# Kernel optimization log

Measured on AMD Instinct MI355X. Metric: run time of the kernel, lower is better.

## Reference

```python
import jax, jax.numpy as jnp
import numpy as np
from jax import lax

B, P, E, H, V, S = 128, 196, 2048, 512, 10000, 21


def setup_inputs() -> dict:
    key = jax.random.key(0)
    ks = jax.random.split(key, 16)
    r = lambda k, shape, s=0.02: (jax.random.normal(k, shape, jnp.float32) * s)
    return {
        "img_features": jax.random.normal(ks[0], (B, P, E), jnp.float32),
        "captions": jax.random.randint(ks[1], (B, S), 0, V),
        "U_w": r(ks[2], (H, H)), "U_b": jnp.zeros((H,), jnp.float32),
        "W_w": r(ks[3], (E, H)), "W_b": jnp.zeros((H,), jnp.float32),
        "v_w": r(ks[4], (H, 1)), "v_b": jnp.zeros((1,), jnp.float32),
        "init_h_w": r(ks[5], (E, H)), "init_h_b": jnp.zeros((H,), jnp.float32),
        "init_c_w": r(ks[6], (E, H)), "init_c_b": jnp.zeros((H,), jnp.float32),
        "f_beta_w": r(ks[7], (H, E)), "f_beta_b": jnp.zeros((E,), jnp.float32),
        "out_w": r(ks[8], (H, V)), "out_b": jnp.zeros((V,), jnp.float32),
        "emb": r(ks[9], (V, H)),
        "lstm_Wih": r(ks[10], (H + E, 4 * H)), "lstm_Whh": r(ks[11], (H, 4 * H)),
        "lstm_bih": jnp.zeros((4 * H,), jnp.float32), "lstm_bhh": jnp.zeros((4 * H,), jnp.float32),
    }


def reference(img_features, captions, U_w, U_b, W_w, W_b, v_w, v_b,
              init_h_w, init_h_b, init_c_w, init_c_b, f_beta_w, f_beta_b,
              out_w, out_b, emb, lstm_Wih, lstm_Whh, lstm_bih, lstm_bhh):
    batch = img_features.shape[0]
    T = captions.shape[1] - 1  # max_timespan (static)

    # init LSTM state from mean-pooled image features
    avg = img_features.mean(axis=1)                       # [B, E]
    h0 = jnp.tanh(avg @ init_h_w + init_h_b)              # [B, H]
    c0 = jnp.tanh(avg @ init_c_w + init_c_b)              # [B, H]

    # precompute W(img_features) once; it does not depend on h
    W_s = img_features @ W_w + W_b                        # [B, P, H]

    # in training mode the original feeds the embedding of word 0 every step
    emb0 = jnp.broadcast_to(emb[0], (batch, emb.shape[1]))  # [B, H]

    def step(carry, _):
        h, c = carry
        # additive attention
        att = jnp.tanh(W_s + (h @ U_w + U_b)[:, None, :])      # [B, P, H]
        e = (att @ v_w)[..., 0] + v_b[0]                        # [B, P]
        alpha = jax.nn.softmax(e, axis=1)                       # [B, P]
        context = jnp.einsum('bp,bpe->be', alpha, img_features) # [B, E]
        # gated context
        gate = jax.nn.sigmoid(h @ f_beta_w + f_beta_b)          # [B, E]
        x = jnp.concatenate([emb0, gate * context], axis=1)     # [B, H+E]
        # LSTMCell (torch gate order i, f, g, o)
        gates = x @ lstm_Wih + lstm_bih + h @ lstm_Whh + lstm_bhh  # [B, 4H]
        i, f, g, o = jnp.split(gates, 4, axis=1)
        i = jax.nn.sigmoid(i); f = jax.nn.sigmoid(f)
        g = jnp.tanh(g); o = jax.nn.sigmoid(o)
        c_new = f * c + i * g
        h_new = o * jnp.tanh(c_new)
        out = h_new @ out_w + out_b                             # [B, V] (dropout = identity, eval)
        return (h_new, c_new), (out, alpha)

    (_, _), (preds, alphas) = lax.scan(step, (h0, c0), None, length=T)
    preds = jnp.transpose(preds, (1, 0, 2))    # [B, T, V]
    alphas = jnp.transpose(alphas, (1, 0, 2))  # [B, T, P]
    return preds, alphas
```

## Files before the change

### kernel.cpp

```cpp
#include <hip/hip_runtime.h>
#include <stdint.h>


typedef unsigned short u16;
typedef unsigned int u32;
typedef __attribute__((ext_vector_type(8))) short bf16x8;
typedef __attribute__((ext_vector_type(4))) float f32x4;

__device__ __forceinline__ float bf2f(u16 u) { return __uint_as_float(((u32)u) << 16); }
__device__ __forceinline__ u16 f2bf(float f) {
  u32 x = __float_as_uint(f);
  u32 r = x + 0x7fffu + ((x >> 16) & 1u);
  return (u16)(r >> 16);
}
__device__ __forceinline__ float tanh_f(float x) {
  x = fminf(15.f, fmaxf(-15.f, x));
  float e = __expf(2.f * x);
  return 1.f - 2.f * __builtin_amdgcn_rcpf(e + 1.f);
}
__device__ __forceinline__ float sigm_f(float x) {
  x = fminf(30.f, fmaxf(-30.f, x));
  return __builtin_amdgcn_rcpf(1.f + __expf(-x));
}

__global__ __launch_bounds__(256) void k_f32_to_bf16(const float* __restrict__ in,
                                                     u16* __restrict__ out) {
  size_t i = ((size_t)blockIdx.x * 256 + threadIdx.x) * 8;
  float4 v0 = *(const float4*)(in + i);
  float4 v1 = *(const float4*)(in + i + 4);
  union { u16 u[8]; uint4 v; } r;
  r.u[0] = f2bf(v0.x); r.u[1] = f2bf(v0.y); r.u[2] = f2bf(v0.z); r.u[3] = f2bf(v0.w);
  r.u[4] = f2bf(v1.x); r.u[5] = f2bf(v1.y); r.u[6] = f2bf(v1.z); r.u[7] = f2bf(v1.w);
  *(uint4*)(out + i) = r.v;
}

__global__ __launch_bounds__(256) void k_avg(const u16* __restrict__ imgb,
                                             u16* __restrict__ avgb) {
  int b = blockIdx.y;
  int c0 = blockIdx.x * 512 + threadIdx.x * 2;
  const u32* p0 = (const u32*)(imgb + (size_t)b * 196 * 2048 + c0);
  float s0 = 0.f, s1 = 0.f;
  for (int p = 0; p < 196; ++p) {
    u32 v = p0[(size_t)p * 1024];
    s0 += bf2f((u16)(v & 0xffff));
    s1 += bf2f((u16)(v >> 16));
  }
  const float inv = 1.f / 196.f;
  u32 o = ((u32)f2bf(s1 * inv) << 16) | (u32)f2bf(s0 * inv);
  *(u32*)(avgb + (size_t)b * 2048 + c0) = o;
}

template <bool PERM>
__global__ __launch_bounds__(256) void k_transpose_bf16(const float* __restrict__ in,
                                                        int R, int C, int Cpad,
                                                        u16* __restrict__ out, int out_ld) {
  __shared__ float tile[32][33];
  int c0 = blockIdx.x * 32, r0 = blockIdx.y * 32;
  int tx = threadIdx.x, ty = threadIdx.y;
#pragma unroll
  for (int i = 0; i < 32; i += 8) {
    int r = r0 + ty + i, c = c0 + tx;
    tile[ty + i][tx] = (r < R && c < C) ? in[(size_t)r * C + c] : 0.f;
  }
  __syncthreads();
#pragma unroll
  for (int i = 0; i < 32; i += 8) {
    int c = c0 + ty + i, r = r0 + tx;
    if (c < Cpad && r < R) {
      int co = PERM ? ((c & 511) * 4 + (c >> 9)) : c;
      out[(size_t)co * out_ld + r] = f2bf(tile[tx][ty + i]);
    }
  }
}

__global__ __launch_bounds__(256) void k_cbias(const float* __restrict__ emb,
                                               const float* __restrict__ Wih,
                                               const float* __restrict__ bih,
                                               const float* __restrict__ bhh,
                                               float* __restrict__ cb) {
  __shared__ float e0[512];
  int tid = threadIdx.x;
  for (int i = tid; i < 512; i += 256) e0[i] = emb[i];
  __syncthreads();
  int n = blockIdx.x * 256 + tid;
  float s = bih[n] + bhh[n];
  for (int k = 0; k < 512; ++k) s += e0[k] * Wih[(size_t)k * 2048 + n];
  cb[(n & 511) * 4 + (n >> 9)] = s;
}

enum { EPI_TANH_H = 0, EPI_TANH_C, EPI_GATE, EPI_LSTM };

template <int EPI>
__global__ __launch_bounds__(256) void k_gemm64(
    const u16* __restrict__ A, const u16* __restrict__ BT, int K, int Ntiles,
    const float* __restrict__ bias, float* __restrict__ outF,
    u16* __restrict__ outB, u16* __restrict__ outB2, u16* __restrict__ outB3,
    const float* __restrict__ ctx, int tstep) {
  __shared__ __align__(16) u16 Asm[64 * 72];
  __shared__ __align__(16) u16 Bsm[64 * 72];
  int bid = blockIdx.x;
  int mt = bid / Ntiles, nt = bid % Ntiles;
  long m0 = (long)mt * 64, n0 = (long)nt * 64;
  int tid = threadIdx.x, lane = tid & 63, w = tid >> 6;
  int srow = tid >> 3, schk = tid & 7;
  f32x4 acc[4] = {};
  const u16* Ap0 = A + (m0 + srow) * K + schk * 8;
  const u16* Ap1 = A + (m0 + srow + 32) * K + schk * 8;
  const u16* Bp0 = BT + (n0 + srow) * K + schk * 8;
  const u16* Bp1 = BT + (n0 + srow + 32) * K + schk * 8;
  u16* Aw0 = Asm + srow * 72 + schk * 8;
  u16* Aw1 = Asm + (srow + 32) * 72 + schk * 8;
  u16* Bw0 = Bsm + srow * 72 + schk * 8;
  u16* Bw1 = Bsm + (srow + 32) * 72 + schk * 8;
  const u16* Ar = Asm + (w * 16 + (lane & 15)) * 72 + (lane >> 4) * 8;
  const u16* Br = Bsm + (lane & 15) * 72 + (lane >> 4) * 8;
  for (int k0 = 0; k0 < K; k0 += 64) {
    uint4 a0 = *(const uint4*)(Ap0 + k0);
    uint4 a1 = *(const uint4*)(Ap1 + k0);
    uint4 b0 = *(const uint4*)(Bp0 + k0);
    uint4 b1 = *(const uint4*)(Bp1 + k0);
    __syncthreads();
    *(uint4*)Aw0 = a0;
    *(uint4*)Aw1 = a1;
    *(uint4*)Bw0 = b0;
    *(uint4*)Bw1 = b1;
    __syncthreads();
#pragma unroll
    for (int kk = 0; kk < 2; ++kk) {
      bf16x8 af = *(const bf16x8*)(Ar + kk * 32);
#pragma unroll
      for (int sn = 0; sn < 4; ++sn) {
        bf16x8 bfr = *(const bf16x8*)(Br + sn * 16 * 72 + kk * 32);
        acc[sn] = __builtin_amdgcn_mfma_f32_16x16x32_bf16(af, bfr, acc[sn], 0, 0, 0);
      }
    }
  }
  int cb = lane & 15, rb = (lane >> 4) * 4;
  if constexpr (EPI == EPI_LSTM) {
    __shared__ float gtile[64][68];
#pragma unroll
    for (int sn = 0; sn < 4; ++sn)
#pragma unroll
      for (int r = 0; r < 4; ++r)
        gtile[w * 16 + rb + r][sn * 16 + cb] = acc[sn][r] + bias[n0 + sn * 16 + cb];
    __syncthreads();
#pragma unroll
    for (int i = 0; i < 4; ++i) {
      int idx = tid * 4 + i;
      int m = idx >> 4, chl = idx & 15;
      float iv = gtile[m][chl * 4 + 0];
      float fv = gtile[m][chl * 4 + 1];
      float gv = gtile[m][chl * 4 + 2];
      float ov = gtile[m][chl * 4 + 3];
      long bg = m0 + m;
      int ch = (int)(n0 >> 2) + chl;
      long ci = bg * 512 + ch;
      float cn = sigm_f(fv) * outF[ci] + sigm_f(iv) * tanh_f(gv);
      float h = sigm_f(ov) * tanh_f(cn);
      outF[ci] = cn;
      u16 hv = f2bf(h);
      outB[ci] = hv;
      outB2[bg * 2560 + 2048 + ch] = hv;
      outB3[((long)tstep * 128 + bg) * 512 + ch] = hv;
    }
  } else {
#pragma unroll
    for (int sn = 0; sn < 4; ++sn) {
#pragma unroll
      for (int r = 0; r < 4; ++r) {
        long m = m0 + w * 16 + rb + r;
        long n = n0 + sn * 16 + cb;
        float v = acc[sn][r];
        if (EPI == EPI_TANH_H) {
          u16 hv = f2bf(tanh_f(v + bias[n]));
          outB[m * 512 + n] = hv;
          outB2[m * 2560 + 2048 + n] = hv;
        } else if (EPI == EPI_TANH_C) {
          outF[m * 512 + n] = tanh_f(v + bias[n]);
        } else {
          outB[m * 2560 + n] = f2bf(sigm_f(v + bias[n]) * ctx[m * 2048 + n]);
        }
      }
    }
  }
}

enum { EPI128_WS = 0, EPI128_OUT };

template <int EPI>
__global__ __launch_bounds__(256) void k_gemm128(
    const u16* __restrict__ A, const u16* __restrict__ BT, int K, int Ntiles,
    const float* __restrict__ bias, float* __restrict__ outF,
    u16* __restrict__ outB, int ncap) {
  __shared__ __align__(16) u16 Asm[128 * 72];
  __shared__ __align__(16) u16 Bsm[128 * 72];
  int bid = blockIdx.x;
  int mt = bid / Ntiles, nt = bid % Ntiles;
  long m0 = (long)mt * 128, n0 = (long)nt * 128;
  int tid = threadIdx.x, lane = tid & 63, w = tid >> 6;
  int wr = w >> 1, wc = w & 1;
  int srow = tid >> 3, schk = tid & 7;
  f32x4 acc[4][4] = {};
  const u16* Ap = A + (m0 + srow) * K + schk * 8;
  const u16* Bp = BT + (n0 + srow) * K + schk * 8;
  u16* Aw = Asm + srow * 72 + schk * 8;
  u16* Bw = Bsm + srow * 72 + schk * 8;
  const u16* Ar = Asm + (wr * 64 + (lane & 15)) * 72 + (lane >> 4) * 8;
  const u16* Br = Bsm + (wc * 64 + (lane & 15)) * 72 + (lane >> 4) * 8;
  for (int k0 = 0; k0 < K; k0 += 64) {
    uint4 a0 = *(const uint4*)(Ap + k0);
    uint4 a1 = *(const uint4*)(Ap + (size_t)32 * K + k0);
    uint4 a2 = *(const uint4*)(Ap + (size_t)64 * K + k0);
    uint4 a3 = *(const uint4*)(Ap + (size_t)96 * K + k0);
    uint4 b0 = *(const uint4*)(Bp + k0);
    uint4 b1 = *(const uint4*)(Bp + (size_t)32 * K + k0);
    uint4 b2 = *(const uint4*)(Bp + (size_t)64 * K + k0);
    uint4 b3 = *(const uint4*)(Bp + (size_t)96 * K + k0);
    __syncthreads();
    *(uint4*)Aw = a0;
    *(uint4*)(Aw + 32 * 72) = a1;
    *(uint4*)(Aw + 64 * 72) = a2;
    *(uint4*)(Aw + 96 * 72) = a3;
    *(uint4*)Bw = b0;
    *(uint4*)(Bw + 32 * 72) = b1;
    *(uint4*)(Bw + 64 * 72) = b2;
    *(uint4*)(Bw + 96 * 72) = b3;
    __syncthreads();
#pragma unroll
    for (int kk = 0; kk < 2; ++kk) {
      bf16x8 af[4], bfv[4];
#pragma unroll
      for (int i = 0; i < 4; ++i) {
        af[i] = *(const bf16x8*)(Ar + i * 16 * 72 + kk * 32);
        bfv[i] = *(const bf16x8*)(Br + i * 16 * 72 + kk * 32);
      }
#pragma unroll
      for (int sm = 0; sm < 4; ++sm)
#pragma unroll
        for (int sn = 0; sn < 4; ++sn)
          acc[sm][sn] = __builtin_amdgcn_mfma_f32_16x16x32_bf16(af[sm], bfv[sn],
                                                                acc[sm][sn], 0, 0, 0);
    }
  }
  int cb = lane & 15, rb = (lane >> 4) * 4;
#pragma unroll
  for (int sm = 0; sm < 4; ++sm) {
#pragma unroll
    for (int sn = 0; sn < 4; ++sn) {
#pragma unroll
      for (int r = 0; r < 4; ++r) {
        long m = m0 + wr * 64 + sm * 16 + rb + r;
        long n = n0 + wc * 64 + sn * 16 + cb;
        float v = acc[sm][sn][r];
        if (EPI == EPI128_WS) {
          outB[m * 512 + n] = f2bf(v + bias[n]);
        } else {
          if (n < ncap) {
            long t = m >> 7, b = m & 127;
            outF[b * 200000 + t * 10000 + n] = v + bias[n];
          }
        }
      }
    }
  }
}

__global__ __launch_bounds__(512) void k_attn_ctx(
    const u16* __restrict__ hb, const u16* __restrict__ UwB,
    const float* __restrict__ U_b, const float* __restrict__ v_w,
    const u16* __restrict__ WsB, const u16* __restrict__ imgb,
    float* __restrict__ ctx, float* __restrict__ alphas_t) {
  int b = blockIdx.x, tid = threadIdx.x, lane = tid & 63, w = tid >> 6;
  __shared__ float h_s[512], hu_s[512], v_s[512], al_s[200];
  h_s[tid] = bf2f(hb[b * 512 + tid]);
  v_s[tid] = v_w[tid];
  __syncthreads();
  {
    float s = U_b[tid];
    const u16* up = UwB + tid;
#pragma unroll 8
    for (int k = 0; k < 512; ++k) s += h_s[k] * bf2f(up[(size_t)k * 512]);
    hu_s[tid] = s;
  }
  __syncthreads();
  for (int p = w; p < 196; p += 8) {
    uint4 pk = *(const uint4*)(WsB + ((size_t)b * 196 + p) * 512 + lane * 8);
    const u16* u = (const u16*)&pk;
    float e = 0.f;
#pragma unroll
    for (int j = 0; j < 8; ++j) {
      int hch = lane * 8 + j;
      e += tanh_f(bf2f(u[j]) + hu_s[hch]) * v_s[hch];
    }
#pragma unroll
    for (int off = 32; off; off >>= 1) e += __shfl_xor(e, off);
    if (lane == 0) al_s[p] = e;
  }
  __syncthreads();
  if (w == 0) {
    float mx = -1e30f;
    for (int q = lane; q < 196; q += 64) mx = fmaxf(mx, al_s[q]);
#pragma unroll
    for (int off = 32; off; off >>= 1) mx = fmaxf(mx, __shfl_xor(mx, off));
    float ssum = 0.f;
    for (int q = lane; q < 196; q += 64) {
      float ex = __expf(al_s[q] - mx);
      al_s[q] = ex;
      ssum += ex;
    }
#pragma unroll
    for (int off = 32; off; off >>= 1) ssum += __shfl_xor(ssum, off);
    float inv = 1.f / ssum;
    for (int q = lane; q < 196; q += 64) al_s[q] *= inv;
  }
  __syncthreads();
  if (tid < 196) alphas_t[(size_t)b * 3920 + tid] = al_s[tid];
  const u32* ib = (const u32*)(imgb + (size_t)b * 196 * 2048) + tid;
  float a0 = 0.f, a1 = 0.f, a2 = 0.f, a3 = 0.f;
#pragma unroll 2
  for (int p = 0; p < 196; ++p) {
    float ap = al_s[p];
    u32 v0 = ib[(size_t)p * 1024];
    u32 v1 = ib[(size_t)p * 1024 + 512];
    a0 += ap * bf2f((u16)(v0 & 0xffff));
    a1 += ap * bf2f((u16)(v0 >> 16));
    a2 += ap * bf2f((u16)(v1 & 0xffff));
    a3 += ap * bf2f((u16)(v1 >> 16));
  }
  float* cp = ctx + (size_t)b * 2048;
  cp[tid * 2] = a0;
  cp[tid * 2 + 1] = a1;
  cp[1024 + tid * 2] = a2;
  cp[1024 + tid * 2 + 1] = a3;
}

extern "C" void kernel_launch(void* const* d_in, const int* in_sizes, int n_in,
                              void* d_out, int out_size, void* d_ws, size_t ws_size,
                              hipStream_t stream) {
  const float* img = (const float*)d_in[0];
  const float* U_w = (const float*)d_in[2];
  const float* U_b = (const float*)d_in[3];
  const float* W_w = (const float*)d_in[4];
  const float* W_b = (const float*)d_in[5];
  const float* v_w = (const float*)d_in[6];
  const float* ih_w = (const float*)d_in[8];
  const float* ih_b = (const float*)d_in[9];
  const float* ic_w = (const float*)d_in[10];
  const float* ic_b = (const float*)d_in[11];
  const float* fb_w = (const float*)d_in[12];
  const float* fb_b = (const float*)d_in[13];
  const float* out_w = (const float*)d_in[14];
  const float* out_b = (const float*)d_in[15];
  const float* emb = (const float*)d_in[16];
  const float* Wih = (const float*)d_in[17];
  const float* Whh = (const float*)d_in[18];
  const float* bih = (const float*)d_in[19];
  const float* bhh = (const float*)d_in[20];
  float* preds = (float*)d_out;
  float* alphas = (float*)d_out + 25600000;

  char* ws = (char*)d_ws;
  size_t off = 0;
  auto alloc = [&](size_t bytes) {
    void* p = ws + off;
    off = (off + bytes + 255) & ~(size_t)255;
    return p;
  };
  u16* imgb = (u16*)alloc((size_t)128 * 196 * 2048 * 2);
  u16* avgb = (u16*)alloc((size_t)128 * 2048 * 2);
  u16* WsB = (u16*)alloc((size_t)128 * 196 * 512 * 2);
  u16* WwT = (u16*)alloc((size_t)512 * 2048 * 2);
  u16* UwB = (u16*)alloc((size_t)512 * 512 * 2);
  u16* ihT = (u16*)alloc((size_t)512 * 2048 * 2);
  u16* icT = (u16*)alloc((size_t)512 * 2048 * 2);
  u16* fbT = (u16*)alloc((size_t)2048 * 512 * 2);
  u16* WcT = (u16*)alloc((size_t)2048 * 2560 * 2);
  u16* owT = (u16*)alloc((size_t)10112 * 512 * 2);
  float* cbias = (float*)alloc(2048 * 4);
  u16* hb = (u16*)alloc((size_t)128 * 512 * 2);
  float* cbuf = (float*)alloc((size_t)128 * 512 * 4);
  float* ctx = (float*)alloc((size_t)128 * 2048 * 4);
  u16* AbufA = (u16*)alloc((size_t)128 * 2560 * 2);
  u16* AbufB = (u16*)alloc((size_t)128 * 2560 * 2);
  u16* hAll = (u16*)alloc((size_t)2560 * 512 * 2);
  if (off > ws_size) return;
  (void)in_sizes; (void)n_in; (void)out_size;

  dim3 tb(32, 8);
  k_f32_to_bf16<<<25088, 256, 0, stream>>>(img, imgb);
  k_f32_to_bf16<<<128, 256, 0, stream>>>(U_w, UwB);
  k_avg<<<dim3(4, 128), 256, 0, stream>>>(imgb, avgb);
  k_transpose_bf16<false><<<dim3(16, 64), tb, 0, stream>>>(W_w, 2048, 512, 512, WwT, 2048);
  k_transpose_bf16<false><<<dim3(16, 64), tb, 0, stream>>>(ih_w, 2048, 512, 512, ihT, 2048);
  k_transpose_bf16<false><<<dim3(16, 64), tb, 0, stream>>>(ic_w, 2048, 512, 512, icT, 2048);
  k_transpose_bf16<false><<<dim3(64, 16), tb, 0, stream>>>(fb_w, 512, 2048, 2048, fbT, 512);
  k_transpose_bf16<false><<<dim3(316, 16), tb, 0, stream>>>(out_w, 512, 10000, 10112, owT, 512);
  k_transpose_bf16<true><<<dim3(64, 64), tb, 0, stream>>>(Wih + 512 * 2048, 2048, 2048, 2048, WcT, 2560);
  k_transpose_bf16<true><<<dim3(64, 16), tb, 0, stream>>>(Whh, 512, 2048, 2048, WcT + 2048, 2560);
  k_cbias<<<8, 256, 0, stream>>>(emb, Wih, bih, bhh, cbias);
  k_gemm128<EPI128_WS><<<784, 256, 0, stream>>>(imgb, WwT, 2048, 4, W_b, nullptr, WsB, 0);
  k_gemm64<EPI_TANH_H><<<16, 256, 0, stream>>>(avgb, ihT, 2048, 8, ih_b, nullptr, hb,
                                               AbufA, nullptr, nullptr, 0);
  k_gemm64<EPI_TANH_C><<<16, 256, 0, stream>>>(avgb, icT, 2048, 8, ic_b, cbuf, nullptr,
                                               nullptr, nullptr, nullptr, 0);

  for (int t = 0; t < 20; ++t) {
    u16* Acur = (t & 1) ? AbufB : AbufA;
    u16* Anxt = (t & 1) ? AbufA : AbufB;
    k_attn_ctx<<<128, 512, 0, stream>>>(hb, UwB, U_b, v_w, WsB, imgb, ctx,
                                        alphas + (size_t)t * 196);
    k_gemm64<EPI_GATE><<<64, 256, 0, stream>>>(hb, fbT, 512, 32, fb_b, nullptr, Acur,
                                               nullptr, nullptr, ctx, 0);
    k_gemm64<EPI_LSTM><<<64, 256, 0, stream>>>(Acur, WcT, 2560, 32, cbias, cbuf, hb,
                                               Anxt, hAll, nullptr, t);
  }
  k_gemm128<EPI128_OUT><<<20 * 79, 256, 0, stream>>>(hAll, owT, 512, 79, out_b,
                                                     preds, nullptr, 10000);
}
```

Baseline: 2.833 ms.

## Merge attention, gate and h@Whh GEMMs into two kernels per timestep

Each timestep's three launches become two. The first kernel runs, in separate blocks, the per-batch attention/context work and an MFMA GEMM of h against a concatenated [f_beta | Whh] weight. The second kernel fuses the sigmoid-gate times context into the A-operand load of the context@Wih GEMM, then adds the precomputed h@Whh and runs the LSTM cell epilogue. Alongside this, the attention path is restructured to use vectorized loads split across waves with shared-memory partial reductions. The aim is fewer launches and less serial latency on the recurrent critical path, at the cost of an fp32 intermediate buffer and sigmoid work recomputed per N-tile.

```diff
diff --git a/kernel.cpp b/kernel.cpp
--- a/kernel.cpp
+++ b/kernel.cpp
@@ -88,14 +88,12 @@
   cb[(n & 511) * 4 + (n >> 9)] = s;
 }
 
-enum { EPI_TANH_H = 0, EPI_TANH_C, EPI_GATE, EPI_LSTM };
+enum { EPI_TANH_H = 0, EPI_TANH_C };
 
 template <int EPI>
 __global__ __launch_bounds__(256) void k_gemm64(
     const u16* __restrict__ A, const u16* __restrict__ BT, int K, int Ntiles,
-    const float* __restrict__ bias, float* __restrict__ outF,
-    u16* __restrict__ outB, u16* __restrict__ outB2, u16* __restrict__ outB3,
-    const float* __restrict__ ctx, int tstep) {
+    const float* __restrict__ bias, float* __restrict__ outF, u16* __restrict__ outB) {
   __shared__ __align__(16) u16 Asm[64 * 72];
   __shared__ __align__(16) u16 Bsm[64 * 72];
   int bid = blockIdx.x;
@@ -136,51 +134,15 @@
     }
   }
   int cb = lane & 15, rb = (lane >> 4) * 4;
-  if constexpr (EPI == EPI_LSTM) {
-    __shared__ float gtile[64][68];
-#pragma unroll
-    for (int sn = 0; sn < 4; ++sn)
-#pragma unroll
-      for (int r = 0; r < 4; ++r)
-        gtile[w * 16 + rb + r][sn * 16 + cb] = acc[sn][r] + bias[n0 + sn * 16 + cb];
-    __syncthreads();
-#pragma unroll
-    for (int i = 0; i < 4; ++i) {
-      int idx = tid * 4 + i;
-      int m = idx >> 4, chl = idx & 15;
-      float iv = gtile[m][chl * 4 + 0];
-      float fv = gtile[m][chl * 4 + 1];
-      float gv = gtile[m][chl * 4 + 2];
-      float ov = gtile[m][chl * 4 + 3];
-      long bg = m0 + m;
-      int ch = (int)(n0 >> 2) + chl;
-      long ci = bg * 512 + ch;
-      float cn = sigm_f(fv) * outF[ci] + sigm_f(iv) * tanh_f(gv);
-      float h = sigm_f(ov) * tanh_f(cn);
-      outF[ci] = cn;
-      u16 hv = f2bf(h);
-      outB[ci] = hv;
-      outB2[bg * 2560 + 2048 + ch] = hv;
-      outB3[((long)tstep * 128 + bg) * 512 + ch] = hv;
-    }
-  } else {
-#pragma unroll
-    for (int sn = 0; sn < 4; ++sn) {
-#pragma unroll
-      for (int r = 0; r < 4; ++r) {
-        long m = m0 + w * 16 + rb + r;
-        long n = n0 + sn * 16 + cb;
-        float v = acc[sn][r];
-        if (EPI == EPI_TANH_H) {
-          u16 hv = f2bf(tanh_f(v + bias[n]));
-          outB[m * 512 + n] = hv;
-          outB2[m * 2560 + 2048 + n] = hv;
-        } else if (EPI == EPI_TANH_C) {
-          outF[m * 512 + n] = tanh_f(v + bias[n]);
-        } else {
-          outB[m * 2560 + n] = f2bf(sigm_f(v + bias[n]) * ctx[m * 2048 + n]);
-        }
-      }
+#pragma unroll
+  for (int sn = 0; sn < 4; ++sn) {
+#pragma unroll
+    for (int r = 0; r < 4; ++r) {
+      long m = m0 + w * 16 + rb + r;
+      long n = n0 + sn * 16 + cb;
+      float v = acc[sn][r] + bias[n];
+      if (EPI == EPI_TANH_H) outB[m * 512 + n] = f2bf(tanh_f(v));
+      else outF[m * 512 + n] = tanh_f(v);
     }
   }
 }
@@ -265,73 +227,257 @@
   }
 }
 
-__global__ __launch_bounds__(512) void k_attn_ctx(
+__global__ __launch_bounds__(256) void k_stepA(
     const u16* __restrict__ hb, const u16* __restrict__ UwB,
     const float* __restrict__ U_b, const float* __restrict__ v_w,
     const u16* __restrict__ WsB, const u16* __restrict__ imgb,
-    float* __restrict__ ctx, float* __restrict__ alphas_t) {
-  int b = blockIdx.x, tid = threadIdx.x, lane = tid & 63, w = tid >> 6;
-  __shared__ float h_s[512], hu_s[512], v_s[512], al_s[200];
-  h_s[tid] = bf2f(hb[b * 512 + tid]);
-  v_s[tid] = v_w[tid];
+    const u16* __restrict__ fWhT, const float* __restrict__ fb_b,
+    float* __restrict__ ctx, float* __restrict__ pre1,
+    float* __restrict__ alphas_t) {
+  __shared__ __align__(16) char smem[46080];
+  int bid = blockIdx.x, tid = threadIdx.x;
+  int lane = tid & 63, w = tid >> 6;
+  if (bid < 128) {
+    int b = bid;
+    float* h_s = (float*)smem;
+    float* v_s = (float*)(smem + 2048);
+    float* p4 = (float*)(smem + 4096);
+    float* al_s = (float*)(smem + 12288);
+    float* ctxp = (float*)(smem + 13312);
+    {
+      u32 hv = *(const u32*)(hb + b * 512 + tid * 2);
+      h_s[tid * 2] = bf2f((u16)(hv & 0xffff));
+      h_s[tid * 2 + 1] = bf2f((u16)(hv >> 16));
+      float2 vv = *(const float2*)(v_w + tid * 2);
+      v_s[tid * 2] = vv.x;
+      v_s[tid * 2 + 1] = vv.y;
+    }
+    __syncthreads();
+    {
+      float acc[8] = {};
+      const u16* up = UwB + (size_t)(w * 128) * 512 + lane * 8;
+#pragma unroll 4
+      for (int k = 0; k < 128; ++k) {
+        float hk = h_s[w * 128 + k];
+        uint4 uv = *(const uint4*)(up + (size_t)k * 512);
+        const u16* uu = (const u16*)&uv;
+#pragma unroll
+        for (int j = 0; j < 8; ++j) acc[j] += hk * bf2f(uu[j]);
+      }
+      float* dst = p4 + w * 512 + lane * 8;
+#pragma unroll
+      for (int j = 0; j < 8; ++j) dst[j] = acc[j];
+    }
+    __syncthreads();
+    {
+      int n = tid * 2;
+#pragma unroll
+      for (int j = 0; j < 2; ++j) {
+        float s = U_b[n + j] + p4[n + j] + p4[512 + n + j] + p4[1024 + n + j] +
+                  p4[1536 + n + j];
+        p4[n + j] = s;
+      }
+    }
+    __syncthreads();
+    const float* hu_s = p4;
+    for (int p = w; p < 196; p += 4) {
+      uint4 pk = *(const uint4*)(WsB + ((size_t)b * 196 + p) * 512 + lane * 8);
+      const u16* uu = (const u16*)&pk;
+      float e = 0.f;
+#pragma unroll
+      for (int j = 0; j < 8; ++j) {
+        int hch = lane * 8 + j;
+        e += tanh_f(bf2f(uu[j]) + hu_s[hch]) * v_s[hch];
+      }
+#pragma unroll
+      for (int off = 32; off; off >>= 1) e += __shfl_xor(e, off);
+      if (lane == 0) al_s[p] = e;
+    }
+    __syncthreads();
+    if (w == 0) {
+      float mx = -1e30f;
+      for (int q = lane; q < 196; q += 64) mx = fmaxf(mx, al_s[q]);
+#pragma unroll
+      for (int off = 32; off; off >>= 1) mx = fmaxf(mx, __shfl_xor(mx, off));
+      float ssum = 0.f;
+      for (int q = lane; q < 196; q += 64) {
+        float ex = __expf(al_s[q] - mx);
+        al_s[q] = ex;
+        ssum += ex;
+      }
+#pragma unroll
+      for (int off = 32; off; off >>= 1) ssum += __shfl_xor(ssum, off);
+      float inv = 1.f / ssum;
+      for (int q = lane; q < 196; q += 64) al_s[q] *= inv;
+    }
+    __syncthreads();
+    if (tid < 196) alphas_t[(size_t)b * 3920 + tid] = al_s[tid];
+    {
+      float a32[32] = {};
+      const u16* ib = imgb + (size_t)b * 196 * 2048 + lane * 32;
+      for (int p = w; p < 196; p += 4) {
+        float ap = al_s[p];
+        const uint4* rp = (const uint4*)(ib + (size_t)p * 2048);
+#pragma unroll
+        for (int q = 0; q < 4; ++q) {
+          uint4 v = rp[q];
+          const u16* uu = (const u16*)&v;
+#pragma unroll
+          for (int j = 0; j < 8; ++j) a32[q * 8 + j] += ap * bf2f(uu[j]);
+        }
+      }
+      float* dst = ctxp + w * 2048 + lane * 32;
+#pragma unroll
+      for (int j = 0; j < 32; ++j) dst[j] = a32[j];
+    }
+    __syncthreads();
+    {
+      int c0 = tid * 8;
+#pragma unroll
+      for (int j = 0; j < 8; ++j) {
+        int c = c0 + j;
+        ctx[(size_t)b * 2048 + c] =
+            ctxp[c] + ctxp[2048 + c] + ctxp[4096 + c] + ctxp[6144 + c];
+      }
+    }
+  } else {
+    u16* Asm = (u16*)smem;
+    u16* Bsm = (u16*)(smem + 9216);
+    int g = bid - 128;
+    int mt = g >> 6, nt = g & 63;
+    long m0 = (long)mt * 64, n0 = (long)nt * 64;
+    int srow = tid >> 3, schk = tid & 7;
+    f32x4 acc[4] = {};
+    const u16* Ap0 = hb + (m0 + srow) * 512 + schk * 8;
+    const u16* Ap1 = hb + (m0 + srow + 32) * 512 + schk * 8;
+    const u16* Bp0 = fWhT + (n0 + srow) * 512 + schk * 8;
+    const u16* Bp1 = fWhT + (n0 + srow + 32) * 512 + schk * 8;
+    u16* Aw0 = Asm + srow * 72 + schk * 8;
+    u16* Aw1 = Asm + (srow + 32) * 72 + schk * 8;
+    u16* Bw0 = Bsm + srow * 72 + schk * 8;
+    u16* Bw1 = Bsm + (srow + 32) * 72 + schk * 8;
+    const u16* Ar = Asm + (w * 16 + (lane & 15)) * 72 + (lane >> 4) * 8;
+    const u16* Br = Bsm + (lane & 15) * 72 + (lane >> 4) * 8;
+#pragma unroll 1
+    for (int k0 = 0; k0 < 512; k0 += 64) {
+      uint4 a0 = *(const uint4*)(Ap0 + k0);
+      uint4 a1 = *(const uint4*)(Ap1 + k0);
+      uint4 b0 = *(const uint4*)(Bp0 + k0);
+      uint4 b1 = *(const uint4*)(Bp1 + k0);
+      __syncthreads();
+      *(uint4*)Aw0 = a0;
+      *(uint4*)Aw1 = a1;
+      *(uint4*)Bw0 = b0;
+      *(uint4*)Bw1 = b1;
+      __syncthreads();
+#pragma unroll
+      for (int kk = 0; kk < 2; ++kk) {
+        bf16x8 af = *(const bf16x8*)(Ar + kk * 32);
+#pragma unroll
+        for (int sn = 0; sn < 4; ++sn) {
+          bf16x8 bfr = *(const bf16x8*)(Br + sn * 16 * 72 + kk * 32);
+          acc[sn] = __builtin_amdgcn_mfma_f32_16x16x32_bf16(af, bfr, acc[sn], 0, 0, 0);
+        }
+      }
+    }
+    int cb = lane & 15, rb = (lane >> 4) * 4;
+#pragma unroll
+    for (int sn = 0; sn < 4; ++sn) {
+#pragma unroll
+      for (int r = 0; r < 4; ++r) {
+        long m = m0 + w * 16 + rb + r;
+        long n = n0 + sn * 16 + cb;
+        float v = acc[sn][r];
+        if (n < 2048) v += fb_b[n];
+        pre1[m * 4096 + n] = v;
+      }
+    }
+  }
+}
+
+__global__ __launch_bounds__(256) void k_stepB(
+    const float* __restrict__ pre1, const float* __restrict__ ctx,
+    const u16* __restrict__ Wc2, const float* __restrict__ cbias,
+    float* __restrict__ cbuf, u16* __restrict__ hb, u16* __restrict__ hAll,
+    int tstep) {
+  __shared__ __align__(16) u16 Asm[32 * 72];
+  __shared__ __align__(16) u16 Bsm[64 * 72];
+  __shared__ float gtile[32][68];
+  int bid = blockIdx.x;
+  int mt = bid >> 5, nt = bid & 31;
+  int m0 = mt * 32, n0 = nt * 64;
+  int tid = threadIdx.x, lane = tid & 63, w = tid >> 6;
+  int arow = tid >> 3, achk = tid & 7;
+  int brow = tid >> 2, bchk = (tid & 3) * 16;
+  f32x4 acc0 = {}, acc1 = {};
+  const float* pA = pre1 + (size_t)(m0 + arow) * 4096 + achk * 8;
+  const float* pC = ctx + (size_t)(m0 + arow) * 2048 + achk * 8;
+  const u16* pB = Wc2 + (size_t)(n0 + brow) * 2048 + bchk;
+  u16* Aw = Asm + arow * 72 + achk * 8;
+  u16* Bw = Bsm + brow * 72 + bchk;
+  const u16* Ar = Asm + (lane & 15) * 72 + (lane >> 4) * 8;
+  const u16* Br = Bsm + (w * 16 + (lane & 15)) * 72 + (lane >> 4) * 8;
+  for (int k0 = 0; k0 < 2048; k0 += 64) {
+    float4 g0 = *(const float4*)(pA + k0);
+    float4 g1 = *(const float4*)(pA + k0 + 4);
+    float4 c0 = *(const float4*)(pC + k0);
+    float4 c1 = *(const float4*)(pC + k0 + 4);
+    uint4 b0 = *(const uint4*)(pB + k0);
+    uint4 b1 = *(const uint4*)(pB + k0 + 8);
+    union { u16 u[8]; uint4 v; } av;
+    av.u[0] = f2bf(sigm_f(g0.x) * c0.x);
+    av.u[1] = f2bf(sigm_f(g0.y) * c0.y);
+    av.u[2] = f2bf(sigm_f(g0.z) * c0.z);
+    av.u[3] = f2bf(sigm_f(g0.w) * c0.w);
+    av.u[4] = f2bf(sigm_f(g1.x) * c1.x);
+    av.u[5] = f2bf(sigm_f(g1.y) * c1.y);
+    av.u[6] = f2bf(sigm_f(g1.z) * c1.z);
+    av.u[7] = f2bf(sigm_f(g1.w) * c1.w);
+    __syncthreads();
+    *(uint4*)Aw = av.v;
+    *(uint4*)Bw = b0;
+    *(uint4*)(Bw + 8) = b1;
+    __syncthreads();
+#pragma unroll
+    for (int kk = 0; kk < 2; ++kk) {
+      bf16x8 a0 = *(const bf16x8*)(Ar + kk * 32);
+      bf16x8 a1 = *(const bf16x8*)(Ar + 16 * 72 + kk * 32);
+      bf16x8 bb = *(const bf16x8*)(Br + kk * 32);
+      acc0 = __builtin_amdgcn_mfma_f32_16x16x32_bf16(a0, bb, acc0, 0, 0, 0);
+      acc1 = __builtin_amdgcn_mfma_f32_16x16x32_bf16(a1, bb, acc1, 0, 0, 0);
+    }
+  }
+  int cbb = lane & 15, rb = (lane >> 4) * 4;
+#pragma unroll
+  for (int s = 0; s < 2; ++s) {
+#pragma unroll
+    for (int r = 0; r < 4; ++r) {
+      int m = s * 16 + rb + r;
+      int nl = w * 16 + cbb;
+      float v = (s ? acc1[r] : acc0[r]) +
+                pre1[(size_t)(m0 + m) * 4096 + 2048 + n0 + nl] + cbias[n0 + nl];
+      gtile[m][nl] = v;
+    }
+  }
   __syncthreads();
-  {
-    float s = U_b[tid];
-    const u16* up = UwB + tid;
-#pragma unroll 8
-    for (int k = 0; k < 512; ++k) s += h_s[k] * bf2f(up[(size_t)k * 512]);
-    hu_s[tid] = s;
-  }
-  __syncthreads();
-  for (int p = w; p < 196; p += 8) {
-    uint4 pk = *(const uint4*)(WsB + ((size_t)b * 196 + p) * 512 + lane * 8);
-    const u16* u = (const u16*)&pk;
-    float e = 0.f;
-#pragma unroll
-    for (int j = 0; j < 8; ++j) {
-      int hch = lane * 8 + j;
-      e += tanh_f(bf2f(u[j]) + hu_s[hch]) * v_s[hch];
-    }
-#pragma unroll
-    for (int off = 32; off; off >>= 1) e += __shfl_xor(e, off);
-    if (lane == 0) al_s[p] = e;
-  }
-  __syncthreads();
-  if (w == 0) {
-    float mx = -1e30f;
-    for (int q = lane; q < 196; q += 64) mx = fmaxf(mx, al_s[q]);
-#pragma unroll
-    for (int off = 32; off; off >>= 1) mx = fmaxf(mx, __shfl_xor(mx, off));
-    float ssum = 0.f;
-    for (int q = lane; q < 196; q += 64) {
-      float ex = __expf(al_s[q] - mx);
-      al_s[q] = ex;
-      ssum += ex;
-    }
-#pragma unroll
-    for (int off = 32; off; off >>= 1) ssum += __shfl_xor(ssum, off);
-    float inv = 1.f / ssum;
-    for (int q = lane; q < 196; q += 64) al_s[q] *= inv;
-  }
-  __syncthreads();
-  if (tid < 196) alphas_t[(size_t)b * 3920 + tid] = al_s[tid];
-  const u32* ib = (const u32*)(imgb + (size_t)b * 196 * 2048) + tid;
-  float a0 = 0.f, a1 = 0.f, a2 = 0.f, a3 = 0.f;
-#pragma unroll 2
-  for (int p = 0; p < 196; ++p) {
-    float ap = al_s[p];
-    u32 v0 = ib[(size_t)p * 1024];
-    u32 v1 = ib[(size_t)p * 1024 + 512];
-    a0 += ap * bf2f((u16)(v0 & 0xffff));
-    a1 += ap * bf2f((u16)(v0 >> 16));
-    a2 += ap * bf2f((u16)(v1 & 0xffff));
-    a3 += ap * bf2f((u16)(v1 >> 16));
-  }
-  float* cp = ctx + (size_t)b * 2048;
-  cp[tid * 2] = a0;
-  cp[tid * 2 + 1] = a1;
-  cp[1024 + tid * 2] = a2;
-  cp[1024 + tid * 2 + 1] = a3;
+#pragma unroll
+  for (int i = 0; i < 2; ++i) {
+    int idx = tid * 2 + i;
+    int m = idx >> 4, chl = idx & 15;
+    float iv = gtile[m][chl * 4 + 0];
+    float fv = gtile[m][chl * 4 + 1];
+    float gv = gtile[m][chl * 4 + 2];
+    float ov = gtile[m][chl * 4 + 3];
+    long bg = m0 + m;
+    int ch = (n0 >> 2) + chl;
+    long ci = bg * 512 + ch;
+    float cn = sigm_f(fv) * cbuf[ci] + sigm_f(iv) * tanh_f(gv);
+    float h = sigm_f(ov) * tanh_f(cn);
+    cbuf[ci] = cn;
+    u16 hv = f2bf(h);
+    hb[ci] = hv;
+    hAll[((size_t)tstep * 128 + bg) * 512 + ch] = hv;
+  }
 }
 
 extern "C" void kernel_launch(void* const* d_in, const int* in_sizes, int n_in,
@@ -373,15 +519,14 @@
   u16* UwB = (u16*)alloc((size_t)512 * 512 * 2);
   u16* ihT = (u16*)alloc((size_t)512 * 2048 * 2);
   u16* icT = (u16*)alloc((size_t)512 * 2048 * 2);
-  u16* fbT = (u16*)alloc((size_t)2048 * 512 * 2);
-  u16* WcT = (u16*)alloc((size_t)2048 * 2560 * 2);
+  u16* fWhT = (u16*)alloc((size_t)4096 * 512 * 2);
+  u16* Wc2 = (u16*)alloc((size_t)2048 * 2048 * 2);
   u16* owT = (u16*)alloc((size_t)10112 * 512 * 2);
   float* cbias = (float*)alloc(2048 * 4);
   u16* hb = (u16*)alloc((size_t)128 * 512 * 2);
   float* cbuf = (float*)alloc((size_t)128 * 512 * 4);
   float* ctx = (float*)alloc((size_t)128 * 2048 * 4);
-  u16* AbufA = (u16*)alloc((size_t)128 * 2560 * 2);
-  u16* AbufB = (u16*)alloc((size_t)128 * 2560 * 2);
+  float* pre1 = (float*)alloc((size_t)128 * 4096 * 4);
   u16* hAll = (u16*)alloc((size_t)2560 * 512 * 2);
   if (off > ws_size) return;
   (void)in_sizes; (void)n_in; (void)out_size;
@@ -393,26 +538,21 @@
   k_transpose_bf16<false><<<dim3(16, 64), tb, 0, stream>>>(W_w, 2048, 512, 512, WwT, 2048);
   k_transpose_bf16<false><<<dim3(16, 64), tb, 0, stream>>>(ih_w, 2048, 512, 512, ihT, 2048);
   k_transpose_bf16<false><<<dim3(16, 64), tb, 0, stream>>>(ic_w, 2048, 512, 512, icT, 2048);
-  k_transpose_bf16<false><<<dim3(64, 16), tb, 0, stream>>>(fb_w, 512, 2048, 2048, fbT, 512);
+  k_transpose_bf16<false><<<dim3(64, 16), tb, 0, stream>>>(fb_w, 512, 2048, 2048, fWhT, 512);
+  k_transpose_bf16<true><<<dim3(64, 16), tb, 0, stream>>>(Whh, 512, 2048, 2048,
+                                                          fWhT + (size_t)2048 * 512, 512);
+  k_transpose_bf16<true><<<dim3(64, 64), tb, 0, stream>>>(Wih + 512 * 2048, 2048, 2048,
+                                                          2048, Wc2, 2048);
   k_transpose_bf16<false><<<dim3(316, 16), tb, 0, stream>>>(out_w, 512, 10000, 10112, owT, 512);
-  k_transpose_bf16<true><<<dim3(64, 64), tb, 0, stream>>>(Wih + 512 * 2048, 2048, 2048, 2048, WcT, 2560);
-  k_transpose_bf16<true><<<dim3(64, 16), tb, 0, stream>>>(Whh, 512, 2048, 2048, WcT + 2048, 2560);
   k_cbias<<<8, 256, 0, stream>>>(emb, Wih, bih, bhh, cbias);
   k_gemm128<EPI128_WS><<<784, 256, 0, stream>>>(imgb, WwT, 2048, 4, W_b, nullptr, WsB, 0);
-  k_gemm64<EPI_TANH_H><<<16, 256, 0, stream>>>(avgb, ihT, 2048, 8, ih_b, nullptr, hb,
-                                               AbufA, nullptr, nullptr, 0);
-  k_gemm64<EPI_TANH_C><<<16, 256, 0, stream>>>(avgb, icT, 2048, 8, ic_b, cbuf, nullptr,
-                                               nullptr, nullptr, nullptr, 0);
+  k_gemm64<EPI_TANH_H><<<16, 256, 0, stream>>>(avgb, ihT, 2048, 8, ih_b, nullptr, hb);
+  k_gemm64<EPI_TANH_C><<<16, 256, 0, stream>>>(avgb, icT, 2048, 8, ic_b, cbuf, nullptr);
 
   for (int t = 0; t < 20; ++t) {
-    u16* Acur = (t & 1) ? AbufB : AbufA;
-    u16* Anxt = (t & 1) ? AbufA : AbufB;
-    k_attn_ctx<<<128, 512, 0, stream>>>(hb, UwB, U_b, v_w, WsB, imgb, ctx,
-                                        alphas + (size_t)t * 196);
-    k_gemm64<EPI_GATE><<<64, 256, 0, stream>>>(hb, fbT, 512, 32, fb_b, nullptr, Acur,
-                                               nullptr, nullptr, ctx, 0);
-    k_gemm64<EPI_LSTM><<<64, 256, 0, stream>>>(Acur, WcT, 2560, 32, cbias, cbuf, hb,
-                                               Anxt, hAll, nullptr, t);
+    k_stepA<<<256, 256, 0, stream>>>(hb, UwB, U_b, v_w, WsB, imgb, fWhT, fb_b, ctx,
+                                     pre1, alphas + (size_t)t * 196);
+    k_stepB<<<128, 256, 0, stream>>>(pre1, ctx, Wc2, cbias, cbuf, hb, hAll, t);
   }
   k_gemm128<EPI128_OUT><<<20 * 79, 256, 0, stream>>>(hAll, owT, 512, 79, out_b,
                                                      preds, nullptr, 10000);
```

Result: faster. 2.517 ms (-11.1%).
